# Performance work log

Measured on AMD Instinct MI355X. Metric: run time of the kernel, lower is better.

The kernel has to match this reference:

```python
import jax, jax.numpy as jnp
import numpy as np

L, H, D, T, DFF, OUT, B = 6, 12, 49, 16, 1024, 10, 8192
STD = 0.02


def setup_inputs() -> dict:
    key = jax.random.key(0)
    ks = jax.random.split(key, 24)
    n = lambda k, shape: jax.random.normal(k, shape, dtype=jnp.float32) * STD
    return {
        "x": jax.random.normal(ks[0], (B, 784), dtype=jnp.float32),
        "mask": jnp.ones((B, T), dtype=bool),  # unused by the original Attention
        # per-layer, per-head Q/K/V/out linears (weights stored as (in, out))
        "Wq": n(ks[1], (L, H, D, D)), "bq": n(ks[2], (L, H, D)),
        "Wk": n(ks[3], (L, H, D, D)), "bk": n(ks[4], (L, H, D)),
        "Wv": n(ks[5], (L, H, D, D)), "bv": n(ks[6], (L, H, D)),
        "Wo": n(ks[7], (L, H, D, D)), "bo": n(ks[8], (L, H, D)),
        # concat projection Linear(D*H, D)
        "Wcat": n(ks[9], (L, H * D, D)), "bcat": n(ks[10], (L, D)),
        # LayerNorms
        "ln1_g": jnp.ones((L, D), jnp.float32), "ln1_b": jnp.zeros((L, D), jnp.float32),
        "ln2_g": jnp.ones((L, D), jnp.float32), "ln2_b": jnp.zeros((L, D), jnp.float32),
        # FeedForward
        "W1": n(ks[11], (L, D, DFF)), "b1": n(ks[12], (L, DFF)),
        "W2": n(ks[13], (L, DFF, D)), "b2": n(ks[14], (L, D)),
        # ClassificationHead
        "Wc": n(ks[15], (D, OUT)), "bc": n(ks[16], (OUT,)),
    }


def _ln(x, g, b):
    mu = jnp.mean(x, axis=-1, keepdims=True)
    var = jnp.mean((x - mu) ** 2, axis=-1, keepdims=True)
    return (x - mu) / jnp.sqrt(var + 1e-5) * g + b


def _forward(x, Wq, bq, Wk, bk, Wv, bv, Wo, bo, Wcat, bcat,
             ln1_g, ln1_b, ln2_g, ln2_b, W1, b1, W2, b2, Wc, bc):
    bsz = x.shape[0]
    h = x.reshape(bsz, T, D)  # MakeTokens
    scale = float(1.0 / np.sqrt(D))
    for i in range(L):
        xn = _ln(h, ln1_g[i], ln1_b[i])
        # all heads batched via einsum (each head attends over full d_model)
        q = jnp.einsum('btd,hde->bhte', xn, Wq[i]) + bq[i][None, :, None, :]
        k = jnp.einsum('btd,hde->bhte', xn, Wk[i]) + bk[i][None, :, None, :]
        v = jnp.einsum('btd,hde->bhte', xn, Wv[i]) + bv[i][None, :, None, :]
        w = jax.nn.softmax(jnp.einsum('bhte,bhse->bhts', q, k) * scale, axis=-1)
        o = jnp.einsum('bhts,bhse->bhte', w, v)
        o = jnp.einsum('bhte,hef->bhtf', o, Wo[i]) + bo[i][None, :, None, :]
        cat = o.transpose(0, 2, 1, 3).reshape(bsz, T, H * D)  # concat heads
        attn = cat @ Wcat[i] + bcat[i]
        x2 = h + attn  # dropout is identity at inference
        xn2 = _ln(x2, ln2_g[i], ln2_b[i])
        ff = jax.nn.relu(xn2 @ W1[i] + b1[i]) @ W2[i] + b2[i]
        h = x2 + ff
    return h[:, 0, :] @ Wc + bc  # ClassificationHead on token 0


def reference(x, mask, Wq, bq, Wk, bk, Wv, bv, Wo, bo, Wcat, bcat,
              ln1_g, ln1_b, ln2_g, ln2_b, W1, b1, W2, b2, Wc, bc):
    # mask is accepted but unused, matching the original Attention.forward
    return _forward(x, Wq, bq, Wk, bk, Wv, bv, Wo, bo, Wcat, bcat,
                    ln1_g, ln1_b, ln2_g, ln2_b, W1, b1, W2, b2, Wc, bc)
```

## Files before the change

### kernel.cpp

```cpp
#include <hip/hip_runtime.h>
#include <hip/hip_bf16.h>

#define LYR 6
#define NH 12
#define DM 49
#define FFD 1024
#define NOUT 10
#define NB 8192
#define NWIN 168
#define SPW 2

typedef __bf16 bf16x8 __attribute__((ext_vector_type(8)));
typedef float f32x4 __attribute__((ext_vector_type(4)));
typedef unsigned int u32;
typedef u32 u32x4 __attribute__((ext_vector_type(4)));

static __device__ __forceinline__ f32x4 mfma_full(u32x4 a, u32x4 b, f32x4 c) {
  return __builtin_amdgcn_mfma_f32_16x16x32_bf16(
      __builtin_bit_cast(bf16x8, a), __builtin_bit_cast(bf16x8, b), c, 0, 0, 0);
}

static __device__ __forceinline__ f32x4 mfma_hz(u32 a0, u32 a1, u32 b0, u32 b1, f32x4 c) {
  u32x4 A = {a0, a1, 0u, 0u};
  u32x4 B = {b0, b1, 0u, 0u};
  return mfma_full(A, B, c);
}

static __device__ __forceinline__ unsigned short f2bf(float f) {
  union { float f; unsigned u; } c; c.f = f;
  unsigned r = c.u + 0x7fffu + ((c.u >> 16) & 1u);
  return (unsigned short)(r >> 16);
}

static __device__ __forceinline__ u32 pk2(float a, float b) {
  __hip_bfloat162 h2 = __float22bfloat162_rn(make_float2(a, b));
  u32 r;
  __builtin_memcpy(&r, &h2, 4);
  return r;
}

static __device__ __forceinline__ void gload16(const void* gp, void* lp) {
  __builtin_amdgcn_global_load_lds(
      (const __attribute__((address_space(1))) unsigned int*)gp,
      (__attribute__((address_space(3))) unsigned int*)lp, 16, 0, 0);
}

static __device__ __forceinline__ void decode(int idx, int& d, int& col) {
  int tile = idx >> 10, ks = (idx >> 9) & 1, lane = (idx >> 3) & 63, j = idx & 7;
  col = 16 * tile + (lane & 15);
  d = 16 * (2 * ks + (j >= 4 ? 1 : 0)) + 4 * (lane >> 4) + (j & 3);
}


__global__ void prep_g_frag(const float* __restrict__ Wq, const float* __restrict__ bq,
                            const float* __restrict__ Wk, const float* __restrict__ bk,
                            unsigned short* __restrict__ blob) {
  const float QS = 1.44269504088896f / 7.0f;
  int lh = blockIdx.x, l = lh / NH, hd = lh % NH;
  unsigned short* base =
      blob + (size_t)(l * 28 + 2 * (hd >> 1)) * 8192 + (hd & 1) * 4096;
  for (int idx = threadIdx.x; idx < 4096; idx += blockDim.x) {
    int kk, cc;
    decode(idx, kk, cc);
    float acc = 0.f;
    if (cc <= DM && kk <= DM) {
      for (int e = 0; e < DM; ++e) {
        float kv = (cc < DM) ? Wk[(size_t)lh * 2401 + cc * DM + e] : bk[lh * DM + e];
        float qv = (kk < DM) ? Wq[(size_t)lh * 2401 + kk * DM + e] : bq[lh * DM + e];
        acc += kv * qv;
      }
      acc *= QS;
    }
    base[idx] = f2bf(acc);
  }
}

__global__ void prep_comb_f32(const float* __restrict__ Wo, const float* __restrict__ bo,
                              const float* __restrict__ Wcat, const float* __restrict__ bcat,
                              float* __restrict__ C) {
  int lh = blockIdx.x, l = lh / NH, hh = lh % NH;
  float* base = C + (size_t)lh * 3200;
  for (int idx = threadIdx.x; idx < 3200; idx += blockDim.x) {
    int e = idx >> 6, f = idx & 63;
    float val = 0.f;
    if (f < DM) {
      if (e < DM) {
        for (int c = 0; c < DM; ++c)
          val += Wo[(size_t)lh * 2401 + e * DM + c] *
                 Wcat[((size_t)l * 588 + hh * DM + c) * DM + f];
      } else {
        for (int c = 0; c < DM; ++c)
          val += bo[lh * DM + c] * Wcat[((size_t)l * 588 + hh * DM + c) * DM + f];
        if (hh == 0) val += bcat[l * DM + f];
      }
    }
    base[idx] = val;
  }
}

__global__ void prep_vc_frag(const float* __restrict__ Wv, const float* __restrict__ bv,
                             const float* __restrict__ C,
                             unsigned short* __restrict__ blob) {
  int lh = blockIdx.x, l = lh / NH, hd = lh % NH;
  const float* Cb = C + (size_t)lh * 3200;
  unsigned short* base =
      blob + (size_t)(l * 28 + 2 * (hd >> 1) + 1) * 8192 + (hd & 1) * 4096;
  for (int idx = threadIdx.x; idx < 4096; idx += blockDim.x) {
    int d, f;
    decode(idx, d, f);
    float acc = 0.f;
    if (f < DM && d <= DM) {
      for (int e = 0; e < DM; ++e) {
        float wv = (d < DM) ? Wv[(size_t)lh * 2401 + d * DM + e] : bv[lh * DM + e];
        acc += wv * Cb[e * 64 + f];
      }
      if (d == DM) acc += Cb[DM * 64 + f];
    }
    base[idx] = f2bf(acc);
  }
}

__global__ void prep_ff_frag(const float* __restrict__ W1, const float* __restrict__ b1,
                             const float* __restrict__ W2,
                             unsigned short* __restrict__ blob) {
  int l = blockIdx.x >> 3, part = blockIdx.x & 7;
  for (int idx = part * 16384 + threadIdx.x; idx < (part + 1) * 16384; idx += blockDim.x) {
    int c = idx >> 13, within = idx & 8191, sec = within >> 12, sidx = within & 4095;
    unsigned short* dst =
        blob + (size_t)(l * 28 + 12 + c) * 8192 + sec * 4096;
    int d, col;
    decode(sidx, d, col);
    float v = 0.f;
    if (sec == 0) {
      int jcol = 64 * c + col;
      if (d < DM) v = W1[(size_t)l * DM * FFD + d * FFD + jcol];
      else if (d == DM) v = b1[l * FFD + jcol];
    } else {
      int jg = 64 * c + d;
      if (col < DM) v = W2[(size_t)l * FFD * DM + jg * DM + col];
    }
    dst[sidx] = f2bf(v);
  }
}

__global__ void prep_small(const float* __restrict__ g1, const float* __restrict__ b1,
                           const float* __restrict__ g2, const float* __restrict__ b2,
                           const float* __restrict__ bff2,
                           float* __restrict__ g1p, float* __restrict__ b1p,
                           float* __restrict__ g2p, float* __restrict__ b2p,
                           float* __restrict__ bff2p) {
  int idx = threadIdx.x;
  if (idx >= 384) return;
  int l = idx >> 6, d = idx & 63;
  bool v = d < DM;
  g1p[idx] = v ? g1[l * DM + d] : 0.f;
  b1p[idx] = v ? b1[l * DM + d] : 0.f;
  g2p[idx] = v ? g2[l * DM + d] : 0.f;
  b2p[idx] = v ? b2[l * DM + d] : 0.f;
  bff2p[idx] = v ? bff2[l * DM + d] : 0.f;
}


static __device__ __forceinline__ void ln_pack(const f32x4 (&h)[4], const f32x4 (&gv)[4],
                                               const f32x4 (&bv)[4], int g, u32x4 (&xf)[2]) {
  float s = 0.f, s2 = 0.f;
#pragma unroll
  for (int mi = 0; mi < 4; ++mi)
#pragma unroll
    for (int r = 0; r < 4; ++r) { float v = h[mi][r]; s += v; s2 += v * v; }
  s += __shfl_xor(s, 16, 64); s += __shfl_xor(s, 32, 64);
  s2 += __shfl_xor(s2, 16, 64); s2 += __shfl_xor(s2, 32, 64);
  float mu = s * (1.f / 49.f);
  float rs = rsqrtf(s2 * (1.f / 49.f) - mu * mu + 1e-5f);
  u32 t[8];
#pragma unroll
  for (int mi = 0; mi < 4; ++mi) {
    float xv[4];
#pragma unroll
    for (int r = 0; r < 4; ++r) xv[r] = (h[mi][r] - mu) * rs * gv[mi][r] + bv[mi][r];
    if (mi == 3) xv[1] = (g == 0) ? 1.0f : xv[1];
    t[2 * mi] = pk2(xv[0], xv[1]);
    t[2 * mi + 1] = pk2(xv[2], xv[3]);
  }
  xf[0] = u32x4{t[0], t[1], t[2], t[3]};
  xf[1] = u32x4{t[4], t[5], t[6], t[7]};
}

static __device__ __forceinline__ void softmax_pk(f32x4 s, u32& p0, u32& p1) {
  float e0 = exp2f(s[0]), e1 = exp2f(s[1]);
  float e2 = exp2f(s[2]), e3 = exp2f(s[3]);
  float su = e0 + e1 + e2 + e3;
  su += __shfl_xor(su, 16, 64);
  su += __shfl_xor(su, 32, 64);
  float inv = 1.f / su;
  p0 = pk2(e0 * inv, e1 * inv);
  p1 = pk2(e2 * inv, e3 * inv);
}

#define STAGE_LOAD(s)                                                         \
  do {                                                                        \
    const unsigned short* gsrc = blob + (size_t)(s) * 8192 + tid * 8;         \
    unsigned short* ldst = &wbuf[(s) & 1][wv * 512];                          \
    _Pragma("unroll") for (int r = 0; r < 4; ++r)                             \
        gload16(gsrc + r * 2048, ldst + r * 2048);                            \
  } while (0)

__global__ __launch_bounds__(256, 4) void transformer_kernel(
    const float* __restrict__ x, float* __restrict__ out,
    const unsigned short* __restrict__ blob,
    const float* __restrict__ lg1, const float* __restrict__ lb1,
    const float* __restrict__ lg2, const float* __restrict__ lb2,
    const float* __restrict__ b2p, const float* __restrict__ Wc,
    const float* __restrict__ bc) {
  __shared__ __align__(16) unsigned short wbuf[2][8192];
  const int tid = threadIdx.x;
  const int wv = tid >> 6, lane = tid & 63;
  const int g = lane >> 4, li = lane & 15;
  const int s0 = blockIdx.x * 8 + wv * 2;
  const f32x4 z4 = {0.f, 0.f, 0.f, 0.f};

  STAGE_LOAD(0);

  f32x4 h[SPW][4];
#pragma unroll
  for (int s = 0; s < SPW; ++s) {
    const float* xa = x + (size_t)(s0 + s) * 784 + li * DM;
#pragma unroll
    for (int mi = 0; mi < 4; ++mi)
#pragma unroll
      for (int r = 0; r < 4; ++r) {
        int d = 16 * mi + 4 * g + r;
        h[s][mi][r] = (d < DM) ? xa[d] : 0.f;
      }
  }

  int w = 0;
  for (int layer = 0; layer < LYR; ++layer) {
    u32x4 xf[SPW][2];
    {
      f32x4 gv[4], bv[4];
#pragma unroll
      for (int mi = 0; mi < 4; ++mi) {
        int off = layer * 64 + 16 * mi + 4 * g;
        gv[mi] = *(const f32x4*)(lg1 + off);
        bv[mi] = *(const f32x4*)(lb1 + off);
      }
#pragma unroll
      for (int s = 0; s < SPW; ++s) ln_pack(h[s], gv, bv, g, xf[s]);
    }

    for (int hp = 0; hp < 6; ++hp) {
      __syncthreads();
      if (w + 1 < NWIN) STAGE_LOAD(w + 1);
      u32 p[2][SPW][2];
#pragma unroll
      for (int hh = 0; hh < 2; ++hh) {
        const u32x4* GW = (const u32x4*)(wbuf[w & 1] + hh * 4096);
        __builtin_amdgcn_s_setprio(1);
        u32x4 yf[SPW][2];
#pragma unroll
        for (int mi = 0; mi < 4; ++mi) {
          f32x4 cy[SPW];
#pragma unroll
          for (int s = 0; s < SPW; ++s) cy[s] = z4;
#pragma unroll
          for (int ks = 0; ks < 2; ++ks) {
            u32x4 gw = GW[(mi * 2 + ks) * 64 + lane];
#pragma unroll
            for (int s = 0; s < SPW; ++s) cy[s] = mfma_full(gw, xf[s][ks], cy[s]);
          }
#pragma unroll
          for (int s = 0; s < SPW; ++s) {
            yf[s][mi >> 1][2 * (mi & 1)] = pk2(cy[s][0], cy[s][1]);
            yf[s][mi >> 1][2 * (mi & 1) + 1] = pk2(cy[s][2], cy[s][3]);
          }
        }
        f32x4 sc[SPW];
#pragma unroll
        for (int s = 0; s < SPW; ++s) {
          sc[s] = mfma_full(xf[s][0], yf[s][0], z4);
          sc[s] = mfma_full(xf[s][1], yf[s][1], sc[s]);
        }
        __builtin_amdgcn_s_setprio(0);
#pragma unroll
        for (int s = 0; s < SPW; ++s) softmax_pk(sc[s], p[hh][s][0], p[hh][s][1]);
      }
      ++w;

      __syncthreads();
      if (w + 1 < NWIN) STAGE_LOAD(w + 1);
#pragma unroll
      for (int hh = 0; hh < 2; ++hh) {
        const u32x4* UW = (const u32x4*)(wbuf[w & 1] + hh * 4096);
        __builtin_amdgcn_s_setprio(1);
#pragma unroll
        for (int nt = 0; nt < 4; ++nt) {
          f32x4 cu[SPW];
#pragma unroll
          for (int s = 0; s < SPW; ++s) cu[s] = z4;
#pragma unroll
          for (int ks = 0; ks < 2; ++ks) {
            u32x4 wu = UW[(nt * 2 + ks) * 64 + lane];
#pragma unroll
            for (int s = 0; s < SPW; ++s) cu[s] = mfma_full(xf[s][ks], wu, cu[s]);
          }
#pragma unroll
          for (int s = 0; s < SPW; ++s) {
            u32 u0 = pk2(cu[s][0], cu[s][1]);
            u32 u1 = pk2(cu[s][2], cu[s][3]);
            h[s][nt] = mfma_hz(u0, u1, p[hh][s][0], p[hh][s][1], h[s][nt]);
          }
        }
        __builtin_amdgcn_s_setprio(0);
      }
      ++w;
    }

    {
      f32x4 gv[4], bv[4];
#pragma unroll
      for (int mi = 0; mi < 4; ++mi) {
        int off = layer * 64 + 16 * mi + 4 * g;
        gv[mi] = *(const f32x4*)(lg2 + off);
        bv[mi] = *(const f32x4*)(lb2 + off);
      }
#pragma unroll
      for (int s = 0; s < SPW; ++s) ln_pack(h[s], gv, bv, g, xf[s]);
#pragma unroll
      for (int mi = 0; mi < 4; ++mi) {
        f32x4 bb = *(const f32x4*)(b2p + layer * 64 + 16 * mi + 4 * g);
#pragma unroll
        for (int s = 0; s < SPW; ++s) h[s][mi] += bb;
      }
    }

    for (int c = 0; c < 16; ++c) {
      __syncthreads();
      if (w + 1 < NWIN) STAGE_LOAD(w + 1);
      const u32x4* W1c = (const u32x4*)wbuf[w & 1];
      const u32x4* W2c = (const u32x4*)(wbuf[w & 1] + 4096);
      __builtin_amdgcn_s_setprio(1);
      u32x4 af[SPW][2];
#pragma unroll
      for (int jt = 0; jt < 4; ++jt) {
        f32x4 ca[SPW];
#pragma unroll
        for (int s = 0; s < SPW; ++s) ca[s] = z4;
#pragma unroll
        for (int ks = 0; ks < 2; ++ks) {
          u32x4 ww = W1c[(jt * 2 + ks) * 64 + lane];
#pragma unroll
          for (int s = 0; s < SPW; ++s) ca[s] = mfma_full(ww, xf[s][ks], ca[s]);
        }
#pragma unroll
        for (int s = 0; s < SPW; ++s) {
          float r0 = fmaxf(ca[s][0], 0.f), r1 = fmaxf(ca[s][1], 0.f);
          float r2 = fmaxf(ca[s][2], 0.f), r3 = fmaxf(ca[s][3], 0.f);
          af[s][jt >> 1][2 * (jt & 1)] = pk2(r0, r1);
          af[s][jt >> 1][2 * (jt & 1) + 1] = pk2(r2, r3);
        }
      }
#pragma unroll
      for (int ft = 0; ft < 4; ++ft) {
#pragma unroll
        for (int ks = 0; ks < 2; ++ks) {
          u32x4 ww = W2c[(ft * 2 + ks) * 64 + lane];
#pragma unroll
          for (int s = 0; s < SPW; ++s) h[s][ft] = mfma_full(ww, af[s][ks], h[s][ft]);
        }
      }
      __builtin_amdgcn_s_setprio(0);
      ++w;
    }
  }

  __syncthreads();
  float* hs = (float*)&wbuf[0][0];
  if (li == 0) {
#pragma unroll
    for (int s = 0; s < SPW; ++s)
#pragma unroll
      for (int mi = 0; mi < 4; ++mi)
#pragma unroll
        for (int r = 0; r < 4; ++r)
          hs[(wv * SPW + s) * 64 + 16 * mi + 4 * g + r] = h[s][mi][r];
  }
  __syncthreads();
  if (lane < 10 * SPW) {
    int smp = lane / 10, c = lane % 10;
    float acc = bc[c];
    const float* hrow = hs + (wv * SPW + smp) * 64;
    for (int d = 0; d < DM; ++d) acc += hrow[d] * Wc[d * NOUT + c];
    out[(size_t)(s0 + smp) * NOUT + c] = acc;
  }
}

extern "C" void kernel_launch(void* const* d_in, const int* in_sizes, int n_in,
                              void* d_out, int out_size, void* d_ws, size_t ws_size,
                              hipStream_t stream) {
  const float* x = (const float*)d_in[0];
  const float* Wq = (const float*)d_in[2];
  const float* bq = (const float*)d_in[3];
  const float* Wk = (const float*)d_in[4];
  const float* bk = (const float*)d_in[5];
  const float* Wv = (const float*)d_in[6];
  const float* bv = (const float*)d_in[7];
  const float* Wo = (const float*)d_in[8];
  const float* bo = (const float*)d_in[9];
  const float* Wcat = (const float*)d_in[10];
  const float* bcat = (const float*)d_in[11];
  const float* ln1_g = (const float*)d_in[12];
  const float* ln1_b = (const float*)d_in[13];
  const float* ln2_g = (const float*)d_in[14];
  const float* ln2_b = (const float*)d_in[15];
  const float* W1 = (const float*)d_in[16];
  const float* b1 = (const float*)d_in[17];
  const float* W2 = (const float*)d_in[18];
  const float* b2 = (const float*)d_in[19];
  const float* Wc = (const float*)d_in[20];
  const float* bc = (const float*)d_in[21];

  unsigned short* blob = (unsigned short*)d_ws;
  float* Cscr = (float*)(blob + (size_t)NWIN * 8192);
  float* fp = Cscr + (size_t)72 * 3200;
  float* g1p = fp;
  float* b1p = g1p + 384;
  float* g2p = b1p + 384;
  float* b2lp = g2p + 384;
  float* b2p = b2lp + 384;

  prep_g_frag<<<72, 256, 0, stream>>>(Wq, bq, Wk, bk, blob);
  prep_comb_f32<<<72, 256, 0, stream>>>(Wo, bo, Wcat, bcat, Cscr);
  prep_vc_frag<<<72, 256, 0, stream>>>(Wv, bv, Cscr, blob);
  prep_ff_frag<<<48, 256, 0, stream>>>(W1, b1, W2, blob);
  prep_small<<<1, 384, 0, stream>>>(ln1_g, ln1_b, ln2_g, ln2_b, b2, g1p, b1p, g2p, b2lp, b2p);

  transformer_kernel<<<NB / 8, 256, 0, stream>>>(
      x, (float*)d_out, blob, g1p, b1p, g2p, b2lp, b2p, Wc, bc);
}
```

Measured before the change: 526.1 us.

## Switch transformer kernel to 32x32x16 MFMA with two-sample groups per wave

Replaces the 16x16x32 bf16 MFMA tiling with 32x32x16 MFMA. Each wave now processes two groups of two samples (32 token rows per tile), so a block uses 2 waves of 128 threads covering 8 samples. Weight fragment layouts in the prep kernels, the layernorm and softmax packing, and the staged LDS loads are all re-derived for the new layout. The aim is fewer, larger matrix instructions and better reuse of each weight fragment. The cost is more accumulator registers per wave and fewer waves per block to hide the per-stage barriers and loads.

```diff
diff --git a/kernel.cpp b/kernel.cpp
--- a/kernel.cpp
+++ b/kernel.cpp
@@ -8,22 +8,17 @@
 #define NOUT 10
 #define NB 8192
 #define NWIN 168
-#define SPW 2
+#define NG 2
 
 typedef __bf16 bf16x8 __attribute__((ext_vector_type(8)));
 typedef float f32x4 __attribute__((ext_vector_type(4)));
+typedef float f32x16 __attribute__((ext_vector_type(16)));
 typedef unsigned int u32;
 typedef u32 u32x4 __attribute__((ext_vector_type(4)));
 
-static __device__ __forceinline__ f32x4 mfma_full(u32x4 a, u32x4 b, f32x4 c) {
-  return __builtin_amdgcn_mfma_f32_16x16x32_bf16(
+static __device__ __forceinline__ f32x16 mfma32(u32x4 a, u32x4 b, f32x16 c) {
+  return __builtin_amdgcn_mfma_f32_32x32x16_bf16(
       __builtin_bit_cast(bf16x8, a), __builtin_bit_cast(bf16x8, b), c, 0, 0, 0);
-}
-
-static __device__ __forceinline__ f32x4 mfma_hz(u32 a0, u32 a1, u32 b0, u32 b1, f32x4 c) {
-  u32x4 A = {a0, a1, 0u, 0u};
-  u32x4 B = {b0, b1, 0u, 0u};
-  return mfma_full(A, B, c);
 }
 
 static __device__ __forceinline__ unsigned short f2bf(float f) {
@@ -45,10 +40,12 @@
       (__attribute__((address_space(3))) unsigned int*)lp, 16, 0, 0);
 }
 
-static __device__ __forceinline__ void decode(int idx, int& d, int& col) {
-  int tile = idx >> 10, ks = (idx >> 9) & 1, lane = (idx >> 3) & 63, j = idx & 7;
-  col = 16 * tile + (lane & 15);
-  d = 16 * (2 * ks + (j >= 4 ? 1 : 0)) + 4 * (lane >> 4) + (j & 3);
+static __device__ __forceinline__ void decode32(int idx, int& k, int& col) {
+  int combo = idx >> 9;
+  int mt = combo >> 2, ks = combo & 3;
+  int lane = (idx >> 3) & 63, j = idx & 7;
+  col = 32 * mt + (lane & 31);
+  k = 16 * ks + 4 * (lane >> 5) + (j & 3) + 8 * (j >> 2);
 }
 
 
@@ -61,7 +58,7 @@
       blob + (size_t)(l * 28 + 2 * (hd >> 1)) * 8192 + (hd & 1) * 4096;
   for (int idx = threadIdx.x; idx < 4096; idx += blockDim.x) {
     int kk, cc;
-    decode(idx, kk, cc);
+    decode32(idx, kk, cc);
     float acc = 0.f;
     if (cc <= DM && kk <= DM) {
       for (int e = 0; e < DM; ++e) {
@@ -107,7 +104,7 @@
       blob + (size_t)(l * 28 + 2 * (hd >> 1) + 1) * 8192 + (hd & 1) * 4096;
   for (int idx = threadIdx.x; idx < 4096; idx += blockDim.x) {
     int d, f;
-    decode(idx, d, f);
+    decode32(idx, d, f);
     float acc = 0.f;
     if (f < DM && d <= DM) {
       for (int e = 0; e < DM; ++e) {
@@ -129,7 +126,7 @@
     unsigned short* dst =
         blob + (size_t)(l * 28 + 12 + c) * 8192 + sec * 4096;
     int d, col;
-    decode(sidx, d, col);
+    decode32(sidx, d, col);
     float v = 0.f;
     if (sec == 0) {
       int jcol = 64 * c + col;
@@ -161,51 +158,65 @@
 }
 
 
-static __device__ __forceinline__ void ln_pack(const f32x4 (&h)[4], const f32x4 (&gv)[4],
-                                               const f32x4 (&bv)[4], int g, u32x4 (&xf)[2]) {
+static __device__ __forceinline__ void ln_pack32(const f32x16 (&ht)[2],
+                                                 const float* gb, const float* bb,
+                                                 int hp5, u32x4 (&xf)[4]) {
   float s = 0.f, s2 = 0.f;
 #pragma unroll
-  for (int mi = 0; mi < 4; ++mi)
-#pragma unroll
-    for (int r = 0; r < 4; ++r) { float v = h[mi][r]; s += v; s2 += v * v; }
-  s += __shfl_xor(s, 16, 64); s += __shfl_xor(s, 32, 64);
-  s2 += __shfl_xor(s2, 16, 64); s2 += __shfl_xor(s2, 32, 64);
+  for (int mt = 0; mt < 2; ++mt)
+#pragma unroll
+    for (int r = 0; r < 16; ++r) { float v = ht[mt][r]; s += v; s2 += v * v; }
+  s += __shfl_xor(s, 32, 64);
+  s2 += __shfl_xor(s2, 32, 64);
   float mu = s * (1.f / 49.f);
   float rs = rsqrtf(s2 * (1.f / 49.f) - mu * mu + 1e-5f);
-  u32 t[8];
-#pragma unroll
-  for (int mi = 0; mi < 4; ++mi) {
-    float xv[4];
-#pragma unroll
-    for (int r = 0; r < 4; ++r) xv[r] = (h[mi][r] - mu) * rs * gv[mi][r] + bv[mi][r];
-    if (mi == 3) xv[1] = (g == 0) ? 1.0f : xv[1];
-    t[2 * mi] = pk2(xv[0], xv[1]);
-    t[2 * mi + 1] = pk2(xv[2], xv[3]);
-  }
-  xf[0] = u32x4{t[0], t[1], t[2], t[3]};
-  xf[1] = u32x4{t[4], t[5], t[6], t[7]};
-}
-
-static __device__ __forceinline__ void softmax_pk(f32x4 s, u32& p0, u32& p1) {
-  float e0 = exp2f(s[0]), e1 = exp2f(s[1]);
-  float e2 = exp2f(s[2]), e3 = exp2f(s[3]);
-  float su = e0 + e1 + e2 + e3;
-  su += __shfl_xor(su, 16, 64);
+  float xn[2][16];
+#pragma unroll
+  for (int mt = 0; mt < 2; ++mt)
+#pragma unroll
+    for (int q = 0; q < 4; ++q) {
+      f32x4 gq = *(const f32x4*)(gb + 32 * mt + 8 * q + 4 * hp5);
+      f32x4 bq = *(const f32x4*)(bb + 32 * mt + 8 * q + 4 * hp5);
+#pragma unroll
+      for (int i = 0; i < 4; ++i)
+        xn[mt][4 * q + i] = (ht[mt][4 * q + i] - mu) * rs * gq[i] + bq[i];
+    }
+  if (hp5 == 0) xn[1][9] = 1.0f;
+#pragma unroll
+  for (int ks = 0; ks < 4; ++ks) {
+    int mt = ks >> 1, rh = ks & 1;
+#pragma unroll
+    for (int w = 0; w < 4; ++w)
+      xf[ks][w] = pk2(xn[mt][rh * 8 + 2 * w], xn[mt][rh * 8 + 2 * w + 1]);
+  }
+}
+
+static __device__ __forceinline__ void softmax32(const f32x16& sc, bool tl16,
+                                                 u32x4& p0, u32x4& p1) {
+  int base = tl16 ? 0 : 8;
+  float e[8];
+  float su = 0.f;
+#pragma unroll
+  for (int i = 0; i < 8; ++i) { e[i] = exp2f(sc[base + i]); su += e[i]; }
   su += __shfl_xor(su, 32, 64);
   float inv = 1.f / su;
-  p0 = pk2(e0 * inv, e1 * inv);
-  p1 = pk2(e2 * inv, e3 * inv);
+  u32x4 v;
+#pragma unroll
+  for (int w = 0; w < 4; ++w) v[w] = pk2(e[2 * w] * inv, e[2 * w + 1] * inv);
+  u32x4 z = {0u, 0u, 0u, 0u};
+  p0 = tl16 ? v : z;
+  p1 = tl16 ? z : v;
 }
 
 #define STAGE_LOAD(s)                                                         \
   do {                                                                        \
     const unsigned short* gsrc = blob + (size_t)(s) * 8192 + tid * 8;         \
     unsigned short* ldst = &wbuf[(s) & 1][wv * 512];                          \
-    _Pragma("unroll") for (int r = 0; r < 4; ++r)                             \
-        gload16(gsrc + r * 2048, ldst + r * 2048);                            \
+    _Pragma("unroll") for (int r = 0; r < 8; ++r)                             \
+        gload16(gsrc + r * 1024, ldst + r * 1024);                            \
   } while (0)
 
-__global__ __launch_bounds__(256, 4) void transformer_kernel(
+__global__ __launch_bounds__(128, 2) void transformer_kernel(
     const float* __restrict__ x, float* __restrict__ out,
     const unsigned short* __restrict__ blob,
     const float* __restrict__ lg1, const float* __restrict__ lb1,
@@ -215,75 +226,72 @@
   __shared__ __align__(16) unsigned short wbuf[2][8192];
   const int tid = threadIdx.x;
   const int wv = tid >> 6, lane = tid & 63;
-  const int g = lane >> 4, li = lane & 15;
-  const int s0 = blockIdx.x * 8 + wv * 2;
-  const f32x4 z4 = {0.f, 0.f, 0.f, 0.f};
+  const int t = lane & 31, hp5 = lane >> 5;
+  const bool tl16 = (lane & 16) == 0;
+  const int s0 = blockIdx.x * 8 + wv * 4;
+  const f32x16 z16 = {0.f, 0.f, 0.f, 0.f, 0.f, 0.f, 0.f, 0.f,
+                      0.f, 0.f, 0.f, 0.f, 0.f, 0.f, 0.f, 0.f};
 
   STAGE_LOAD(0);
 
-  f32x4 h[SPW][4];
-#pragma unroll
-  for (int s = 0; s < SPW; ++s) {
-    const float* xa = x + (size_t)(s0 + s) * 784 + li * DM;
-#pragma unroll
-    for (int mi = 0; mi < 4; ++mi)
-#pragma unroll
-      for (int r = 0; r < 4; ++r) {
-        int d = 16 * mi + 4 * g + r;
-        h[s][mi][r] = (d < DM) ? xa[d] : 0.f;
+  f32x16 h[NG][2];
+#pragma unroll
+  for (int grp = 0; grp < NG; ++grp) {
+    int smp = s0 + grp * 2 + (t >> 4);
+    const float* xa = x + (size_t)smp * 784 + (t & 15) * DM;
+#pragma unroll
+    for (int mt = 0; mt < 2; ++mt)
+#pragma unroll
+      for (int r = 0; r < 16; ++r) {
+        int f = (r & 3) + 8 * (r >> 2) + 4 * hp5 + 32 * mt;
+        h[grp][mt][r] = (f < DM) ? xa[f] : 0.f;
       }
   }
 
   int w = 0;
   for (int layer = 0; layer < LYR; ++layer) {
-    u32x4 xf[SPW][2];
-    {
-      f32x4 gv[4], bv[4];
-#pragma unroll
-      for (int mi = 0; mi < 4; ++mi) {
-        int off = layer * 64 + 16 * mi + 4 * g;
-        gv[mi] = *(const f32x4*)(lg1 + off);
-        bv[mi] = *(const f32x4*)(lb1 + off);
-      }
-#pragma unroll
-      for (int s = 0; s < SPW; ++s) ln_pack(h[s], gv, bv, g, xf[s]);
-    }
+    u32x4 xf[NG][4];
+#pragma unroll
+    for (int grp = 0; grp < NG; ++grp)
+      ln_pack32(h[grp], lg1 + layer * 64, lb1 + layer * 64, hp5, xf[grp]);
 
     for (int hp = 0; hp < 6; ++hp) {
       __syncthreads();
       if (w + 1 < NWIN) STAGE_LOAD(w + 1);
-      u32 p[2][SPW][2];
+      u32x4 pB[2][NG][2];
 #pragma unroll
       for (int hh = 0; hh < 2; ++hh) {
         const u32x4* GW = (const u32x4*)(wbuf[w & 1] + hh * 4096);
         __builtin_amdgcn_s_setprio(1);
-        u32x4 yf[SPW][2];
-#pragma unroll
-        for (int mi = 0; mi < 4; ++mi) {
-          f32x4 cy[SPW];
-#pragma unroll
-          for (int s = 0; s < SPW; ++s) cy[s] = z4;
-#pragma unroll
-          for (int ks = 0; ks < 2; ++ks) {
-            u32x4 gw = GW[(mi * 2 + ks) * 64 + lane];
-#pragma unroll
-            for (int s = 0; s < SPW; ++s) cy[s] = mfma_full(gw, xf[s][ks], cy[s]);
+        f32x16 cy[NG][2];
+#pragma unroll
+        for (int grp = 0; grp < NG; ++grp) { cy[grp][0] = z16; cy[grp][1] = z16; }
+#pragma unroll
+        for (int mt = 0; mt < 2; ++mt)
+#pragma unroll
+          for (int ks = 0; ks < 4; ++ks) {
+            u32x4 gw = GW[(mt * 4 + ks) * 64 + lane];
+#pragma unroll
+            for (int grp = 0; grp < NG; ++grp)
+              cy[grp][mt] = mfma32(gw, xf[grp][ks], cy[grp][mt]);
           }
 #pragma unroll
-          for (int s = 0; s < SPW; ++s) {
-            yf[s][mi >> 1][2 * (mi & 1)] = pk2(cy[s][0], cy[s][1]);
-            yf[s][mi >> 1][2 * (mi & 1) + 1] = pk2(cy[s][2], cy[s][3]);
+        for (int grp = 0; grp < NG; ++grp) {
+          u32x4 yB[4];
+#pragma unroll
+          for (int ks = 0; ks < 4; ++ks) {
+            int mt = ks >> 1, rh = ks & 1;
+#pragma unroll
+            for (int ww = 0; ww < 4; ++ww)
+              yB[ks][ww] = pk2(cy[grp][mt][rh * 8 + 2 * ww],
+                               cy[grp][mt][rh * 8 + 2 * ww + 1]);
           }
-        }
-        f32x4 sc[SPW];
-#pragma unroll
-        for (int s = 0; s < SPW; ++s) {
-          sc[s] = mfma_full(xf[s][0], yf[s][0], z4);
-          sc[s] = mfma_full(xf[s][1], yf[s][1], sc[s]);
+          f32x16 sc = z16;
+#pragma unroll
+          for (int ks = 0; ks < 4; ++ks) sc = mfma32(xf[grp][ks], yB[ks], sc);
+          softmax32(sc, tl16, pB[hh][grp][0], pB[hh][grp][1]);
         }
         __builtin_amdgcn_s_setprio(0);
-#pragma unroll
-        for (int s = 0; s < SPW; ++s) softmax_pk(sc[s], p[hh][s][0], p[hh][s][1]);
       }
       ++w;
 
@@ -293,46 +301,50 @@
       for (int hh = 0; hh < 2; ++hh) {
         const u32x4* UW = (const u32x4*)(wbuf[w & 1] + hh * 4096);
         __builtin_amdgcn_s_setprio(1);
-#pragma unroll
-        for (int nt = 0; nt < 4; ++nt) {
-          f32x4 cu[SPW];
-#pragma unroll
-          for (int s = 0; s < SPW; ++s) cu[s] = z4;
-#pragma unroll
-          for (int ks = 0; ks < 2; ++ks) {
-            u32x4 wu = UW[(nt * 2 + ks) * 64 + lane];
-#pragma unroll
-            for (int s = 0; s < SPW; ++s) cu[s] = mfma_full(xf[s][ks], wu, cu[s]);
+        f32x16 cu[NG][2];
+#pragma unroll
+        for (int grp = 0; grp < NG; ++grp) { cu[grp][0] = z16; cu[grp][1] = z16; }
+#pragma unroll
+        for (int nt = 0; nt < 2; ++nt)
+#pragma unroll
+          for (int ks = 0; ks < 4; ++ks) {
+            u32x4 wu = UW[(nt * 4 + ks) * 64 + lane];
+#pragma unroll
+            for (int grp = 0; grp < NG; ++grp)
+              cu[grp][nt] = mfma32(xf[grp][ks], wu, cu[grp][nt]);
           }
 #pragma unroll
-          for (int s = 0; s < SPW; ++s) {
-            u32 u0 = pk2(cu[s][0], cu[s][1]);
-            u32 u1 = pk2(cu[s][2], cu[s][3]);
-            h[s][nt] = mfma_hz(u0, u1, p[hh][s][0], p[hh][s][1], h[s][nt]);
+        for (int grp = 0; grp < NG; ++grp)
+#pragma unroll
+          for (int nt = 0; nt < 2; ++nt) {
+#pragma unroll
+            for (int kss = 0; kss < 2; ++kss) {
+              u32x4 uB;
+#pragma unroll
+              for (int ww = 0; ww < 4; ++ww)
+                uB[ww] = pk2(cu[grp][nt][kss * 8 + 2 * ww],
+                             cu[grp][nt][kss * 8 + 2 * ww + 1]);
+              h[grp][nt] = mfma32(uB, pB[hh][grp][kss], h[grp][nt]);
+            }
           }
-        }
         __builtin_amdgcn_s_setprio(0);
       }
       ++w;
     }
 
-    {
-      f32x4 gv[4], bv[4];
-#pragma unroll
-      for (int mi = 0; mi < 4; ++mi) {
-        int off = layer * 64 + 16 * mi + 4 * g;
-        gv[mi] = *(const f32x4*)(lg2 + off);
-        bv[mi] = *(const f32x4*)(lb2 + off);
-      }
-#pragma unroll
-      for (int s = 0; s < SPW; ++s) ln_pack(h[s], gv, bv, g, xf[s]);
-#pragma unroll
-      for (int mi = 0; mi < 4; ++mi) {
-        f32x4 bb = *(const f32x4*)(b2p + layer * 64 + 16 * mi + 4 * g);
-#pragma unroll
-        for (int s = 0; s < SPW; ++s) h[s][mi] += bb;
-      }
-    }
+#pragma unroll
+    for (int grp = 0; grp < NG; ++grp)
+      ln_pack32(h[grp], lg2 + layer * 64, lb2 + layer * 64, hp5, xf[grp]);
+#pragma unroll
+    for (int mt = 0; mt < 2; ++mt)
+#pragma unroll
+      for (int q = 0; q < 4; ++q) {
+        f32x4 bb = *(const f32x4*)(b2p + layer * 64 + 32 * mt + 8 * q + 4 * hp5);
+#pragma unroll
+        for (int grp = 0; grp < NG; ++grp)
+#pragma unroll
+          for (int i = 0; i < 4; ++i) h[grp][mt][4 * q + i] += bb[i];
+      }
 
     for (int c = 0; c < 16; ++c) {
       __syncthreads();
@@ -340,35 +352,39 @@
       const u32x4* W1c = (const u32x4*)wbuf[w & 1];
       const u32x4* W2c = (const u32x4*)(wbuf[w & 1] + 4096);
       __builtin_amdgcn_s_setprio(1);
-      u32x4 af[SPW][2];
-#pragma unroll
-      for (int jt = 0; jt < 4; ++jt) {
-        f32x4 ca[SPW];
-#pragma unroll
-        for (int s = 0; s < SPW; ++s) ca[s] = z4;
-#pragma unroll
-        for (int ks = 0; ks < 2; ++ks) {
-          u32x4 ww = W1c[(jt * 2 + ks) * 64 + lane];
-#pragma unroll
-          for (int s = 0; s < SPW; ++s) ca[s] = mfma_full(ww, xf[s][ks], ca[s]);
+      f32x16 ca[NG][2];
+#pragma unroll
+      for (int grp = 0; grp < NG; ++grp) { ca[grp][0] = z16; ca[grp][1] = z16; }
+#pragma unroll
+      for (int jt = 0; jt < 2; ++jt)
+#pragma unroll
+        for (int ks = 0; ks < 4; ++ks) {
+          u32x4 w1 = W1c[(jt * 4 + ks) * 64 + lane];
+#pragma unroll
+          for (int grp = 0; grp < NG; ++grp)
+            ca[grp][jt] = mfma32(w1, xf[grp][ks], ca[grp][jt]);
         }
-#pragma unroll
-        for (int s = 0; s < SPW; ++s) {
-          float r0 = fmaxf(ca[s][0], 0.f), r1 = fmaxf(ca[s][1], 0.f);
-          float r2 = fmaxf(ca[s][2], 0.f), r3 = fmaxf(ca[s][3], 0.f);
-          af[s][jt >> 1][2 * (jt & 1)] = pk2(r0, r1);
-          af[s][jt >> 1][2 * (jt & 1) + 1] = pk2(r2, r3);
+      u32x4 aB[NG][4];
+#pragma unroll
+      for (int grp = 0; grp < NG; ++grp)
+#pragma unroll
+        for (int ks = 0; ks < 4; ++ks) {
+          int jt = ks >> 1, rh = ks & 1;
+#pragma unroll
+          for (int ww = 0; ww < 4; ++ww)
+            aB[grp][ks][ww] =
+                pk2(fmaxf(ca[grp][jt][rh * 8 + 2 * ww], 0.f),
+                    fmaxf(ca[grp][jt][rh * 8 + 2 * ww + 1], 0.f));
         }
-      }
-#pragma unroll
-      for (int ft = 0; ft < 4; ++ft) {
-#pragma unroll
-        for (int ks = 0; ks < 2; ++ks) {
-          u32x4 ww = W2c[(ft * 2 + ks) * 64 + lane];
-#pragma unroll
-          for (int s = 0; s < SPW; ++s) h[s][ft] = mfma_full(ww, af[s][ks], h[s][ft]);
+#pragma unroll
+      for (int ft = 0; ft < 2; ++ft)
+#pragma unroll
+        for (int ks = 0; ks < 4; ++ks) {
+          u32x4 w2 = W2c[(ft * 4 + ks) * 64 + lane];
+#pragma unroll
+          for (int grp = 0; grp < NG; ++grp)
+            h[grp][ft] = mfma32(w2, aB[grp][ks], h[grp][ft]);
         }
-      }
       __builtin_amdgcn_s_setprio(0);
       ++w;
     }
@@ -376,20 +392,25 @@
 
   __syncthreads();
   float* hs = (float*)&wbuf[0][0];
-  if (li == 0) {
-#pragma unroll
-    for (int s = 0; s < SPW; ++s)
-#pragma unroll
-      for (int mi = 0; mi < 4; ++mi)
-#pragma unroll
-        for (int r = 0; r < 4; ++r)
-          hs[(wv * SPW + s) * 64 + 16 * mi + 4 * g + r] = h[s][mi][r];
+  if ((lane & 15) == 0) {
+    int sw = (lane >> 4) & 1;
+#pragma unroll
+    for (int grp = 0; grp < NG; ++grp) {
+      int si = wv * 4 + grp * 2 + sw;
+#pragma unroll
+      for (int mt = 0; mt < 2; ++mt)
+#pragma unroll
+        for (int r = 0; r < 16; ++r) {
+          int f = (r & 3) + 8 * (r >> 2) + 4 * hp5 + 32 * mt;
+          hs[si * 64 + f] = h[grp][mt][r];
+        }
+    }
   }
   __syncthreads();
-  if (lane < 10 * SPW) {
+  if (lane < 40) {
     int smp = lane / 10, c = lane % 10;
     float acc = bc[c];
-    const float* hrow = hs + (wv * SPW + smp) * 64;
+    const float* hrow = hs + (wv * 4 + smp) * 64;
     for (int d = 0; d < DM; ++d) acc += hrow[d] * Wc[d * NOUT + c];
     out[(size_t)(s0 + smp) * NOUT + c] = acc;
   }
@@ -435,6 +456,6 @@
   prep_ff_frag<<<48, 256, 0, stream>>>(W1, b1, W2, blob);
   prep_small<<<1, 384, 0, stream>>>(ln1_g, ln1_b, ln2_g, ln2_b, b2, g1p, b1p, g2p, b2lp, b2p);
 
-  transformer_kernel<<<NB / 8, 256, 0, stream>>>(
+  transformer_kernel<<<NB / 8, 128, 0, stream>>>(
       x, (float*)d_out, blob, g1p, b1p, g2p, b2lp, b2p, Wc, bc);
 }
```

Measured after the change: 699.8 us. +33.0%, slower.
